# Kernel tuning notes

Hardware: AMD Instinct MI355X
Metric: run time of the kernel (lower is better)

The kernel has to match this reference:

```python
import jax, jax.numpy as jnp
import numpy as np

GRID = 0.5
N_GRID = (48, 48, 48)
K = 14  # max bbox extent: floor(2 + 2*1.5*1.7/0.5) + 1 = 13, +1 slack
E2 = float(np.exp(2.0))


def _splat(vecs, r):
    """Scatter-add per-atom vdW kernels into a (48,48,48) grid. vecs: [N,3]."""
    ngf = jnp.asarray(N_GRID, jnp.float32)
    ngi = jnp.asarray(N_GRID, jnp.int32)
    vec = vecs + ngf * 0.5 - 0.5                      # [N,3] shifted coords
    b = 1.5 * r
    # int() in torch truncates toward zero; astype(int32) matches, and the
    # clip to [0, n_grid] makes the negative-value difference irrelevant.
    min_pt = jnp.clip(((vec - b) / GRID).astype(jnp.int32), 0, ngi)   # [N,3]
    max_pt = jnp.clip((2.0 + (vec + b) / GRID).astype(jnp.int32), 0, ngi)
    offs = jnp.arange(K, dtype=jnp.int32)
    idx = min_pt[:, None, :] + offs[None, :, None]    # [N,K,3]
    valid = idx < max_pt[:, None, :]                  # [N,K,3] (idx >= min_pt >= 0)
    dax = vec[:, None, :] - GRID * idx.astype(jnp.float32)  # [N,K,3]
    d2ax = dax * dax
    # dense per-atom distance blocks [N,K,K,K]
    d2 = (d2ax[:, :, None, None, 0]
          + d2ax[:, None, :, None, 1]
          + d2ax[:, None, None, :, 2])
    d = jnp.sqrt(d2)
    r2 = r * r
    f1 = jnp.exp(-2.0 * d2 / r2)
    f2 = 4.0 * d2 / (E2 * r2) - 12.0 * d / (E2 * r) + 9.0 / E2
    val = jnp.where(d < r, f1, jnp.where(d < 1.5 * r, f2, 0.0))
    m = (valid[:, :, None, None, 0]
         & valid[:, None, :, None, 1]
         & valid[:, None, None, :, 2])
    val = jnp.where(m, val, 0.0)
    ic = jnp.minimum(idx, ngi - 1)                    # keep indices in-bounds (masked anyway)
    out = jnp.zeros(N_GRID, jnp.float32)
    return out.at[ic[:, :, None, None, 0],
                  ic[:, None, :, None, 1],
                  ic[:, None, None, :, 2]].add(val)


def setup_inputs() -> dict:
    key = jax.random.key(0)
    kC, kN, kO = jax.random.split(key, 3)
    N = 16384
    # atoms uniform inside the 24A box centered at origin
    mk = lambda k: jax.random.uniform(k, (N, 3), jnp.float32, -12.0, 12.0)
    return {"vecs_C": mk(kC), "vecs_N": mk(kN), "vecs_O": mk(kO)}


def reference(vecs_C, vecs_N, vecs_O):
    return jnp.stack([_splat(vecs_C, 1.7),
                      _splat(vecs_N, 1.55),
                      _splat(vecs_O, 1.52)], axis=0)  # [3,48,48,48]
```

## Files before the change

### kernel.cpp

```cpp
#include <hip/hip_runtime.h>

#define NG 48
#define NT 6
#define NTILES (NT * NT * NT)
#define CAP 1536
#define MAXSEG 8
#define LISTS_OFF  8192
#define COPIES_OFF (2u << 20)

__device__ __forceinline__ float type_r(int type) {
    return (type == 0) ? 1.7f : ((type == 1) ? 1.55f : 1.52f);
}

__global__ __launch_bounds__(256) void bin_kernel(
    const float* __restrict__ vC, const float* __restrict__ vN,
    const float* __restrict__ vO, int* __restrict__ cnt,
    unsigned short* __restrict__ lists, int natoms)
{
    const int type = blockIdx.y;
    const float r = type_r(type);
    const float b = 1.5f * r + 1e-3f;
    const float* __restrict__ vecs = (type == 0) ? vC : ((type == 1) ? vN : vO);
    const int tid  = threadIdx.x;
    const int atom = blockIdx.x * 256 + tid;

    __shared__ int lcnt[NTILES];
    __shared__ int lbase[NTILES];
    __shared__ int lfill[NTILES];
    if (tid < NTILES) { lcnt[tid] = 0; lfill[tid] = 0; }
    __syncthreads();

    int x0 = 1, x1 = 0, y0 = 1, y1 = 0, z0 = 1, z1 = 0;
    if (atom < natoms) {
        const float vx = vecs[3 * atom + 0] + 23.5f;
        const float vy = vecs[3 * atom + 1] + 23.5f;
        const float vz = vecs[3 * atom + 2] + 23.5f;
        x0 = max(0,      (int)floorf((vx - 3.5f - b) * 0.25f) + 1);
        x1 = min(NT - 1, (int)ceilf ((vx + b)        * 0.25f) - 1);
        y0 = max(0,      (int)floorf((vy - 3.5f - b) * 0.25f) + 1);
        y1 = min(NT - 1, (int)ceilf ((vy + b)        * 0.25f) - 1);
        z0 = max(0,      (int)floorf((vz - 3.5f - b) * 0.25f) + 1);
        z1 = min(NT - 1, (int)ceilf ((vz + b)        * 0.25f) - 1);
    }
    const bool has = (x0 <= x1) & (y0 <= y1) & (z0 <= z1);

    if (has)
        for (int tx = x0; tx <= x1; ++tx)
            for (int ty = y0; ty <= y1; ++ty)
                for (int tz = z0; tz <= z1; ++tz)
                    atomicAdd(&lcnt[(tx * NT + ty) * NT + tz], 1);
    __syncthreads();

    if (tid < NTILES && lcnt[tid] > 0)
        lbase[tid] = atomicAdd(&cnt[type * NTILES + tid], lcnt[tid]);
    __syncthreads();

    if (has)
        for (int tx = x0; tx <= x1; ++tx)
            for (int ty = y0; ty <= y1; ++ty)
                for (int tz = z0; tz <= z1; ++tz) {
                    const int tl = (tx * NT + ty) * NT + tz;
                    const int p  = lbase[tl] + atomicAdd(&lfill[tl], 1);
                    if (p < CAP)
                        lists[(size_t)(type * NTILES + tl) * CAP + p] =
                            (unsigned short)atom;
                }
}

__global__ __launch_bounds__(256) void gather_seg(
    const float* __restrict__ vC, const float* __restrict__ vN,
    const float* __restrict__ vO, const int* __restrict__ cnt,
    const unsigned short* __restrict__ lists, float* __restrict__ copies,
    int nseg)
{
    const int type = blockIdx.y;
    const float r = type_r(type);
    const float* __restrict__ vecs = (type == 0) ? vC : ((type == 1) ? vN : vO);

    const int s = blockIdx.x / NTILES;
    const int t = blockIdx.x - s * NTILES;
    const int tx = t / (NT * NT);
    const int ty = (t / NT) % NT;
    const int tz = t % NT;

    const int lt  = type * NTILES + t;
    const int n   = min(cnt[lt], CAP);
    const int len = (n + nseg - 1) / nseg;
    const int start = s * len;
    const int end   = min(n, start + len);
    if (start >= end) return;

    const int tid = threadIdx.x;
    const int lx  = tid >> 6;
    const int ly  = (tid >> 3) & 7;
    const int lz  = tid & 7;

    const float b      = 1.5f * r;
    const float r15sq  = b * b;
    const float rr     = r * r;
    const float E2     = 7.3890562f;
    const float c2a    = 4.0f / (E2 * rr);
    const float c2b    = 12.0f / (E2 * r);
    const float c2c    = 9.0f / E2;
    const float n2orr  = -2.0f / rr;

    const float px0 = 0.5f * (float)(tx * 8 + lx);
    const float px1 = px0 + 2.0f;
    const float py  = 0.5f * (float)(ty * 8 + ly);
    const float pz  = 0.5f * (float)(tz * 8 + lz);

    __shared__ float4 sa[256];
    const unsigned short* __restrict__ lst = lists + (size_t)lt * CAP;

    float acc0 = 0.0f, acc1 = 0.0f;

    for (int base = start; base < end; base += 256) {
        const int m = min(256, end - base);
        if (tid < m) {
            const int idx = (int)lst[base + tid];
            sa[tid] = make_float4(vecs[3 * idx + 0] + 23.5f,
                                  vecs[3 * idx + 1] + 23.5f,
                                  vecs[3 * idx + 2] + 23.5f, 0.0f);
        }
        __syncthreads();

        for (int j = 0; j < m; ++j) {
            const float4 a = sa[j];
            const float dy  = a.y - py;
            const float dz  = a.z - pz;
            const float syz = fmaf(dy, dy, dz * dz);
            const float dx0 = a.x - px0;
            const float d2a = fmaf(dx0, dx0, syz);
            const float dx1 = a.x - px1;
            const float d2b = fmaf(dx1, dx1, syz);
            const bool h0 = d2a < r15sq;
            const bool h1 = d2b < r15sq;
            if (__ballot(h0 | h1) == 0ull) continue;
            if (h0) {
                const float d = sqrtf(d2a);
                acc0 += (d < r) ? __expf(n2orr * d2a)
                                : fmaf(c2a, d2a, fmaf(-c2b, d, c2c));
            }
            if (h1) {
                const float d = sqrtf(d2b);
                acc1 += (d < r) ? __expf(n2orr * d2b)
                                : fmaf(c2a, d2b, fmaf(-c2b, d, c2c));
            }
        }
        __syncthreads();
    }

    float* __restrict__ cp = copies + ((size_t)lt * MAXSEG + s) * 512;
    cp[tid]       = acc0;
    cp[tid + 256] = acc1;
}

__global__ __launch_bounds__(256) void reduce_kernel(
    const int* __restrict__ cnt, const float* __restrict__ copies,
    float* __restrict__ out, int nseg)
{
    const int type = blockIdx.y;
    const int t = blockIdx.x;
    const int tx = t / (NT * NT);
    const int ty = (t / NT) % NT;
    const int tz = t % NT;
    const int tid = threadIdx.x;
    const int lx  = tid >> 6;
    const int ly  = (tid >> 3) & 7;
    const int lz  = tid & 7;

    const int lt  = type * NTILES + t;
    const int n   = min(cnt[lt], CAP);
    const int len = (n + nseg - 1) / nseg;
    const float* __restrict__ cp = copies + ((size_t)lt * MAXSEG) * 512;

    float o0 = 0.0f, o1 = 0.0f;
    for (int ss = 0; ss < nseg; ++ss) {
        if (ss * len >= n) break;
        o0 += cp[(size_t)ss * 512 + tid];
        o1 += cp[(size_t)ss * 512 + 256 + tid];
    }

    const int X0 = tx * 8 + lx;
    const int Y  = ty * 8 + ly;
    const int Z  = tz * 8 + lz;
    float* __restrict__ o = out + (size_t)type * NG * NG * NG;
    o[((X0      * NG) + Y) * NG + Z] = o0;
    o[(((X0 + 4) * NG) + Y) * NG + Z] = o1;
}

extern "C" void kernel_launch(void* const* d_in, const int* in_sizes, int n_in,
                              void* d_out, int out_size, void* d_ws, size_t ws_size,
                              hipStream_t stream) {
    const float* vC = (const float*)d_in[0];
    const float* vN = (const float*)d_in[1];
    const float* vO = (const float*)d_in[2];
    float* out = (float*)d_out;

    int* cnt = (int*)d_ws;
    unsigned short* lists = (unsigned short*)((char*)d_ws + LISTS_OFF);
    float* copies = (float*)((char*)d_ws + COPIES_OFF);

    const size_t copy_bytes = (size_t)3 * NTILES * MAXSEG * 512 * sizeof(float);
    int nseg = (ws_size >= COPIES_OFF + copy_bytes) ? MAXSEG : 4;

    const int natoms = in_sizes[0] / 3;

    hipMemsetAsync(cnt, 0, 3 * NTILES * sizeof(int), stream);

    dim3 bgrid((natoms + 255) / 256, 3, 1);
    bin_kernel<<<bgrid, 256, 0, stream>>>(vC, vN, vO, cnt, lists, natoms);

    dim3 ggrid(NTILES * nseg, 3, 1);
    gather_seg<<<ggrid, 256, 0, stream>>>(vC, vN, vO, cnt, lists, copies, nseg);

    dim3 rgrid(NTILES, 3, 1);
    reduce_kernel<<<rgrid, 256, 0, stream>>>(cnt, copies, out, nseg);
}
```

Before: 44.47 us.

## Compute 2x2 grid points per thread in gather and enlarge bin blocks

The gather kernel now has each thread cover four grid points (two x by two z offsets), sharing the dy and dz partial sums. It runs 128-thread blocks and unrolls the atom loop by two. This is meant to cut per-point arithmetic and shared-memory reads per atom, at the cost of fewer waves per tile, more registers and coarser ballot skipping. The binning kernel also moves to 512-thread blocks to halve global atomics per tile. The reduce kernel index mapping is updated to match the new copy layout.

```diff
diff --git a/kernel.cpp b/kernel.cpp
--- a/kernel.cpp
+++ b/kernel.cpp
@@ -12,7 +12,7 @@
     return (type == 0) ? 1.7f : ((type == 1) ? 1.55f : 1.52f);
 }
 
-__global__ __launch_bounds__(256) void bin_kernel(
+__global__ __launch_bounds__(512) void bin_kernel(
     const float* __restrict__ vC, const float* __restrict__ vN,
     const float* __restrict__ vO, int* __restrict__ cnt,
     unsigned short* __restrict__ lists, int natoms)
@@ -22,7 +22,7 @@
     const float b = 1.5f * r + 1e-3f;
     const float* __restrict__ vecs = (type == 0) ? vC : ((type == 1) ? vN : vO);
     const int tid  = threadIdx.x;
-    const int atom = blockIdx.x * 256 + tid;
+    const int atom = blockIdx.x * 512 + tid;
 
     __shared__ int lcnt[NTILES];
     __shared__ int lbase[NTILES];
@@ -67,7 +67,41 @@
                 }
 }
 
-__global__ __launch_bounds__(256) void gather_seg(
+#define EVAL_ATOM(a)                                                         \
+    {                                                                        \
+        const float dy   = (a).y - py;                                       \
+        const float sy   = dy * dy;                                          \
+        const float dz0  = (a).z - pz0;                                      \
+        const float dz1  = (a).z - pz1;                                      \
+        const float syz0 = fmaf(dz0, dz0, sy);                               \
+        const float syz1 = fmaf(dz1, dz1, sy);                               \
+        const float dx0  = (a).x - px0;                                      \
+        const float dx1  = (a).x - px1;                                      \
+        const float xx0  = dx0 * dx0;                                        \
+        const float xx1  = dx1 * dx1;                                        \
+        const float d200 = syz0 + xx0;                                       \
+        const float d201 = syz1 + xx0;                                       \
+        const float d210 = syz0 + xx1;                                       \
+        const float d211 = syz1 + xx1;                                       \
+        const bool h00 = d200 < r15sq, h01 = d201 < r15sq;                   \
+        const bool h10 = d210 < r15sq, h11 = d211 < r15sq;                   \
+        if (__ballot(h00 | h01 | h10 | h11) != 0ull) {                       \
+            if (h00) { const float d = sqrtf(d200);                          \
+                acc00 += (d < r) ? __expf(n2orr * d200)                      \
+                                 : fmaf(c2a, d200, fmaf(-c2b, d, c2c)); }    \
+            if (h01) { const float d = sqrtf(d201);                          \
+                acc01 += (d < r) ? __expf(n2orr * d201)                      \
+                                 : fmaf(c2a, d201, fmaf(-c2b, d, c2c)); }    \
+            if (h10) { const float d = sqrtf(d210);                          \
+                acc10 += (d < r) ? __expf(n2orr * d210)                      \
+                                 : fmaf(c2a, d210, fmaf(-c2b, d, c2c)); }    \
+            if (h11) { const float d = sqrtf(d211);                          \
+                acc11 += (d < r) ? __expf(n2orr * d211)                      \
+                                 : fmaf(c2a, d211, fmaf(-c2b, d, c2c)); }    \
+        }                                                                    \
+    }
+
+__global__ __launch_bounds__(128) void gather_seg(
     const float* __restrict__ vC, const float* __restrict__ vN,
     const float* __restrict__ vO, const int* __restrict__ cnt,
     const unsigned short* __restrict__ lists, float* __restrict__ copies,
@@ -79,9 +113,6 @@
 
     const int s = blockIdx.x / NTILES;
     const int t = blockIdx.x - s * NTILES;
-    const int tx = t / (NT * NT);
-    const int ty = (t / NT) % NT;
-    const int tz = t % NT;
 
     const int lt  = type * NTILES + t;
     const int n   = min(cnt[lt], CAP);
@@ -90,10 +121,14 @@
     const int end   = min(n, start + len);
     if (start >= end) return;
 
+    const int tx = t / (NT * NT);
+    const int ty = (t / NT) % NT;
+    const int tz = t % NT;
+
     const int tid = threadIdx.x;
-    const int lx  = tid >> 6;
-    const int ly  = (tid >> 3) & 7;
-    const int lz  = tid & 7;
+    const int lx  = tid >> 5;
+    const int ly  = (tid >> 2) & 7;
+    const int lz  = tid & 3;
 
     const float b      = 1.5f * r;
     const float r15sq  = b * b;
@@ -107,15 +142,16 @@
     const float px0 = 0.5f * (float)(tx * 8 + lx);
     const float px1 = px0 + 2.0f;
     const float py  = 0.5f * (float)(ty * 8 + ly);
-    const float pz  = 0.5f * (float)(tz * 8 + lz);
-
-    __shared__ float4 sa[256];
+    const float pz0 = 0.5f * (float)(tz * 8 + lz);
+    const float pz1 = pz0 + 2.0f;
+
+    __shared__ float4 sa[128];
     const unsigned short* __restrict__ lst = lists + (size_t)lt * CAP;
 
-    float acc0 = 0.0f, acc1 = 0.0f;
-
-    for (int base = start; base < end; base += 256) {
-        const int m = min(256, end - base);
+    float acc00 = 0.0f, acc01 = 0.0f, acc10 = 0.0f, acc11 = 0.0f;
+
+    for (int base = start; base < end; base += 128) {
+        const int m = min(128, end - base);
         if (tid < m) {
             const int idx = (int)lst[base + tid];
             sa[tid] = make_float4(vecs[3 * idx + 0] + 23.5f,
@@ -124,35 +160,29 @@
         }
         __syncthreads();
 
-        for (int j = 0; j < m; ++j) {
-            const float4 a = sa[j];
-            const float dy  = a.y - py;
-            const float dz  = a.z - pz;
-            const float syz = fmaf(dy, dy, dz * dz);
-            const float dx0 = a.x - px0;
-            const float d2a = fmaf(dx0, dx0, syz);
-            const float dx1 = a.x - px1;
-            const float d2b = fmaf(dx1, dx1, syz);
-            const bool h0 = d2a < r15sq;
-            const bool h1 = d2b < r15sq;
-            if (__ballot(h0 | h1) == 0ull) continue;
-            if (h0) {
-                const float d = sqrtf(d2a);
-                acc0 += (d < r) ? __expf(n2orr * d2a)
-                                : fmaf(c2a, d2a, fmaf(-c2b, d, c2c));
-            }
-            if (h1) {
-                const float d = sqrtf(d2b);
-                acc1 += (d < r) ? __expf(n2orr * d2b)
-                                : fmaf(c2a, d2b, fmaf(-c2b, d, c2c));
-            }
+        int j = 0;
+        for (; j + 1 < m; j += 2) {
+            const float4 a0 = sa[j];
+            const float4 a1 = sa[j + 1];
+            EVAL_ATOM(a0);
+            EVAL_ATOM(a1);
+        }
+        if (j < m) {
+            const float4 a0 = sa[j];
+            EVAL_ATOM(a0);
         }
         __syncthreads();
     }
 
     float* __restrict__ cp = copies + ((size_t)lt * MAXSEG + s) * 512;
-    cp[tid]       = acc0;
-    cp[tid + 256] = acc1;
+    const int c00 = ((lx      * 8) + ly) * 8 + lz;
+    const int c01 = ((lx      * 8) + ly) * 8 + lz + 4;
+    const int c10 = (((lx + 4) * 8) + ly) * 8 + lz;
+    const int c11 = (((lx + 4) * 8) + ly) * 8 + lz + 4;
+    cp[c00] = acc00;
+    cp[c01] = acc01;
+    cp[c10] = acc10;
+    cp[c11] = acc11;
 }
 
 __global__ __launch_bounds__(256) void reduce_kernel(
@@ -165,7 +195,7 @@
     const int ty = (t / NT) % NT;
     const int tz = t % NT;
     const int tid = threadIdx.x;
-    const int lx  = tid >> 6;
+    const int lx0 = tid >> 6;
     const int ly  = (tid >> 3) & 7;
     const int lz  = tid & 7;
 
@@ -174,14 +204,17 @@
     const int len = (n + nseg - 1) / nseg;
     const float* __restrict__ cp = copies + ((size_t)lt * MAXSEG) * 512;
 
+    const int c0 = ((lx0      * 8) + ly) * 8 + lz;
+    const int c1 = (((lx0 + 4) * 8) + ly) * 8 + lz;
+
     float o0 = 0.0f, o1 = 0.0f;
     for (int ss = 0; ss < nseg; ++ss) {
         if (ss * len >= n) break;
-        o0 += cp[(size_t)ss * 512 + tid];
-        o1 += cp[(size_t)ss * 512 + 256 + tid];
-    }
-
-    const int X0 = tx * 8 + lx;
+        o0 += cp[(size_t)ss * 512 + c0];
+        o1 += cp[(size_t)ss * 512 + c1];
+    }
+
+    const int X0 = tx * 8 + lx0;
     const int Y  = ty * 8 + ly;
     const int Z  = tz * 8 + lz;
     float* __restrict__ o = out + (size_t)type * NG * NG * NG;
@@ -208,11 +241,11 @@
 
     hipMemsetAsync(cnt, 0, 3 * NTILES * sizeof(int), stream);
 
-    dim3 bgrid((natoms + 255) / 256, 3, 1);
-    bin_kernel<<<bgrid, 256, 0, stream>>>(vC, vN, vO, cnt, lists, natoms);
+    dim3 bgrid((natoms + 511) / 512, 3, 1);
+    bin_kernel<<<bgrid, 512, 0, stream>>>(vC, vN, vO, cnt, lists, natoms);
 
     dim3 ggrid(NTILES * nseg, 3, 1);
-    gather_seg<<<ggrid, 256, 0, stream>>>(vC, vN, vO, cnt, lists, copies, nseg);
+    gather_seg<<<ggrid, 128, 0, stream>>>(vC, vN, vO, cnt, lists, copies, nseg);
 
     dim3 rgrid(NTILES, 3, 1);
     reduce_kernel<<<rgrid, 256, 0, stream>>>(cnt, copies, out, nseg);
```

Result: slower. 45.62 us (+2.6%).
